# Kernel optimization log

Measured on AMD Instinct MI355X. Metric: run time of the kernel, lower is better.

The kernel has to match this reference:

```python
import jax, jax.numpy as jnp
import numpy as np
import math

B, C, N, T = 16, 32, 500, 10
NH, DK = 8, 8
D = NH * DK  # 64
TT = 6       # tem_size after conv_temp1 (10->6)
EPS = 1e-5


def setup_inputs() -> dict:
    key = jax.random.key(0)
    ks = jax.random.split(key, 32)
    s = 0.05
    rn = lambda k, shp: jax.random.normal(k, shp, dtype=jnp.float32) * s
    return {
        "x": jax.random.normal(ks[0], (B, C, N, T), dtype=jnp.float32),
        "A": jax.random.uniform(ks[1], (N, N), dtype=jnp.float32) / N,
        "conv1_W": rn(ks[2], (32, 32)), "conv1_b": jnp.zeros((32,), jnp.float32),
        "te1_W": rn(ks[3], (64, 32)), "te1_b": jnp.zeros((64,), jnp.float32),
        "convq_W": rn(ks[4], (64, 64, 1, 3)), "convq_b": jnp.zeros((64,), jnp.float32),
        "convk_W": rn(ks[5], (64, 64, 1, 3)), "convk_b": jnp.zeros((64,), jnp.float32),
        "linv_W": rn(ks[6], (64, 64)), "linv_b": jnp.zeros((64,), jnp.float32),
        "lino_W": rn(ks[7], (64, 64)), "lino_b": jnp.zeros((64,), jnp.float32),
        "te2_W": rn(ks[8], (32, 64)), "te2_b": jnp.zeros((32,), jnp.float32),
        "mlp_W": rn(ks[9], (64, 160)), "mlp_b": jnp.zeros((64,), jnp.float32),
        "ct1_W": rn(ks[10], (6, 10)), "ct1_b": jnp.zeros((6,), jnp.float32),
        "tat_c1_W": rn(ks[11], (32,)), "tat_c2_W": rn(ks[12], (500,)),
        "tat_w": rn(ks[13], (500, 32)), "tat_b": jnp.zeros((6, 6), jnp.float32),
        "tat_v": rn(ks[14], (6, 6)),
        "bn1_g": jnp.ones((6,), jnp.float32), "bn1_b": jnp.zeros((6,), jnp.float32),
        "bn2_g": jnp.ones((32,), jnp.float32), "bn2_b": jnp.zeros((32,), jnp.float32),
    }


def _forward(x, A, conv1_W, conv1_b, te1_W, te1_b, convq_W, convq_b, convk_W, convk_b,
             linv_W, linv_b, lino_W, lino_b, te2_W, te2_b, mlp_W, mlp_b, ct1_W, ct1_b,
             tat_c1_W, tat_c2_W, tat_w, tat_b, tat_v, bn1_g, bn1_b, bn2_g, bn2_b):
    b, c, n, t = x.shape
    c1x1 = lambda z, W, bb: jnp.einsum('bchw,oc->bohw', z, W) + bb[None, :, None, None]
    residual = c1x1(x, conv1_W, conv1_b)                      # (B,32,N,T)
    h = c1x1(x, te1_W, te1_b)                                 # (B,64,N,T)
    # --- temporal-context multi-head self-attention (att bias is 0 in source due to bug) ---
    dn = ('NCHW', 'OIHW', 'NCHW')
    q = jax.lax.conv_general_dilated(h, convq_W, (1, 1), ((0, 0), (1, 1)), dimension_numbers=dn) + convq_b[None, :, None, None]
    k = jax.lax.conv_general_dilated(h, convk_W, (1, 1), ((0, 0), (1, 1)), dimension_numbers=dn) + convk_b[None, :, None, None]
    sh = lambda z: z.reshape(b, NH, DK, n, t).transpose(0, 3, 1, 4, 2)  # (B,N,h,T,dk)
    q, k = sh(q), sh(k)
    hp = h.transpose(0, 2, 3, 1)                              # (B,N,T,64)
    v = (hp @ linv_W.T + linv_b).reshape(b, n, t, NH, DK).transpose(0, 1, 3, 2, 4)
    p = jax.nn.softmax(jnp.einsum('bnhtd,bnhsd->bnhts', q, k) / math.sqrt(DK), axis=-1)
    o = jnp.einsum('bnhts,bnhsd->bnhtd', p, v).transpose(0, 1, 3, 2, 4).reshape(b, n, t, D)
    h = (o @ lino_W.T + lino_b).transpose(0, 3, 1, 2)         # (B,64,N,T)
    h = c1x1(h, te2_W, te2_b)                                 # (B,32,N,T)
    # --- multi_gcn_d: static adjacency diffusion + per-timestep attention adjacency ---
    co = h.shape[1]
    xt = h.transpose(0, 3, 2, 1)                              # (B,T,N,C)
    att = jax.nn.softmax(jnp.einsum('btnc,btmc->btnm', xt, xt) / math.sqrt(co), axis=-1)
    outs = [h]
    z = jnp.einsum('btvc,wv->btwc', xt, A); outs.append(z.transpose(0, 3, 2, 1))
    z = jnp.einsum('btvc,wv->btwc', z, A);  outs.append(z.transpose(0, 3, 2, 1))
    z = jnp.einsum('btvc,btwv->btwc', xt, att); outs.append(z.transpose(0, 3, 2, 1))
    z = jnp.einsum('btvc,btwv->btwc', z, att);  outs.append(z.transpose(0, 3, 2, 1))
    hc = c1x1(jnp.concatenate(outs, axis=1), mlp_W, mlp_b)    # (B,64,N,T)
    g = jnp.tanh(hc[:, :co]) * jax.nn.sigmoid(hc[:, co:])     # (B,32,N,10)
    # --- conv_temp1: 1x1 conv over the time axis, 10 -> 6 ---
    g = jnp.einsum('bcnt,st->bcns', g, ct1_W) + ct1_b[None, None, None, :]  # (B,32,N,6)
    # --- TATT_1 temporal attention coefficients ---
    f1 = jnp.einsum('bcnt,c->btn', g, tat_c1_W)               # (B,6,N)
    f2 = jnp.einsum('bcnt,n->bct', g, tat_c2_W)               # (B,32,6)
    logits = jax.nn.sigmoid(jnp.einsum('btn,nc,bcs->bts', f1, tat_w, f2) + tat_b)
    logits = jnp.einsum('pt,bts->bps', tat_v, logits)         # (B,6,6)
    lp = logits.transpose(0, 2, 1)
    mu = lp.mean((0, 2), keepdims=True); var = lp.var((0, 2), keepdims=True)
    lp = (lp - mu) / jnp.sqrt(var + EPS) * bn1_g[None, :, None] + bn1_b[None, :, None]
    coefs = jax.nn.softmax(lp.transpose(0, 2, 1), axis=-1)    # (B,6,6)
    Tc = coefs.transpose(0, 2, 1)
    xo = jnp.einsum('bcnl,blq->bcnq', g, Tc)                  # (B,32,N,6)
    xo = jnp.where(xo > 0, xo, 0.01 * xo) + residual[..., -xo.shape[-1]:]
    mu = xo.mean((0, 2, 3), keepdims=True); var = xo.var((0, 2, 3), keepdims=True)
    return (xo - mu) / jnp.sqrt(var + EPS) * bn2_g[None, :, None, None] + bn2_b[None, :, None, None]


def reference(x, A, conv1_W, conv1_b, te1_W, te1_b, convq_W, convq_b, convk_W, convk_b,
              linv_W, linv_b, lino_W, lino_b, te2_W, te2_b, mlp_W, mlp_b, ct1_W, ct1_b,
              tat_c1_W, tat_c2_W, tat_w, tat_b, tat_v, bn1_g, bn1_b, bn2_g, bn2_b):
    return _forward(x, A, conv1_W, conv1_b, te1_W, te1_b, convq_W, convq_b, convk_W, convk_b,
                    linv_W, linv_b, lino_W, lino_b, te2_W, te2_b, mlp_W, mlp_b, ct1_W, ct1_b,
                    tat_c1_W, tat_c2_W, tat_w, tat_b, tat_v, bn1_g, bn1_b, bn2_g, bn2_b)
```

## Files before the change

### kernel.cpp

```cpp
#include <hip/hip_runtime.h>

typedef unsigned short u16;
typedef unsigned int u32;

__device__ __forceinline__ float b2f(u16 v) { return __uint_as_float((u32)v << 16); }
__device__ __forceinline__ float lopart(u32 u) { return __uint_as_float(u << 16); }
__device__ __forceinline__ float hipart(u32 u) { return __uint_as_float(u & 0xffff0000u); }
__device__ __forceinline__ u16 f2b(float f) {
  u32 u = __float_as_uint(f);
  u32 r = u + 0x7fffu + ((u >> 16) & 1u);
  return (u16)(r >> 16);
}
__device__ __forceinline__ u32 pk2(float a, float b) {
  return (u32)f2b(a) | ((u32)f2b(b) << 16);
}
__device__ __forceinline__ u32 cvtpk(float lo, float hi) {
  u32 r;
  asm("v_cvt_pk_bf16_f32 %0, %1, %2" : "=v"(r) : "v"(lo), "v"(hi));
  return r;
}
__device__ __forceinline__ float rd(const void* p, int i, bool BF) {
  return BF ? b2f(((const u16*)p)[i]) : ((const float*)p)[i];
}

struct Ptrs { const void* p[29]; };

typedef __attribute__((ext_vector_type(8))) short short8;
typedef __attribute__((ext_vector_type(4))) float floatx4;

__global__ __launch_bounds__(256) void k_prep(Ptrs ps, float* __restrict__ Wf,
                                              u16* __restrict__ Abf, float* __restrict__ WT,
                                              u16* __restrict__ WBu, float* __restrict__ stats) {
  bool BF = ((*(const u32*)ps.p[25]) & 0xffffu) != 0;
  int blk = blockIdx.x, tid = threadIdx.x;
  if (blk < 256) {
    int j = blk * 256 + tid;
    if (j >= 65322) return;
    const int SZ[27] = {1024,32,2048,64,12288,64,12288,64,4096,64,4096,64,2048,32,
                        10240,64,60,6,32,500,16000,36,36,6,6,32,32};
    int t = 0, off = 0;
#pragma unroll
    for (int k = 0; k < 27; ++k) {
      if (t == k && j >= off + SZ[k]) { off += SZ[k]; t = k + 1; }
    }
    Wf[j] = rd(ps.p[2 + t], j - off, BF);
  } else if (blk < 1280) {
    int i = (blk - 256) * 256 + tid;
    int r = i >> 9, v = i & 511;
    bool in = (r < 500) && (v < 500);
    u16 o = 0;
    if (in) o = BF ? ((const u16*)ps.p[1])[r * 500 + v] : f2b(((const float*)ps.p[1])[r * 500 + v]);
    Abf[i] = o;
  } else if (blk < 1366) {
    int i = (blk - 1280) * 256 + tid;
    const void* p2  = ps.p[2];
    const void* p4  = ps.p[4];
    const void* p5  = ps.p[5];
    const void* p6  = ps.p[6];
    const void* p7  = ps.p[7];
    const void* p8  = ps.p[8];
    const void* p9  = ps.p[9];
    const void* p10 = ps.p[10];
    const void* p11 = ps.p[11];
    const void* p12 = ps.p[12];
    const void* p13 = ps.p[13];
    const void* p14 = ps.p[14];
    const void* p15 = ps.p[15];
    const void* p16 = ps.p[16];
    if (i < 1024) {
      WT[i] = rd(p2, (i & 31) * 32 + (i >> 5), BF);
    } else if (i < 7168) {
      int j2 = i - 1024;
      int o = j2 & 63, ct = j2 >> 6;
      int c = ct / 3, tap = ct - c * 3;
      float sq = 0.f, sk = 0.f;
      for (int i2 = 0; i2 < 64; ++i2) {
        float te = rd(p4, i2 * 32 + c, BF);
        sq += rd(p6, o * 192 + i2 * 3 + tap, BF) * te;
        sk += rd(p8, o * 192 + i2 * 3 + tap, BF) * te;
      }
      ((u32*)WT)[i] = pk2(sq, sk);
    } else if (i < 7552) {
      int j2 = i - 7168;
      int f = j2 >> 6, o = j2 & 63;
      const void* pw = (f & 1) ? p8 : p6;
      float S0 = 0.f, S1 = 0.f, S2 = 0.f;
      for (int i2 = 0; i2 < 64; ++i2) {
        float tb = rd(p5, i2, BF);
        S0 += rd(pw, o * 192 + i2 * 3 + 0, BF) * tb;
        S1 += rd(pw, o * 192 + i2 * 3 + 1, BF) * tb;
        S2 += rd(pw, o * 192 + i2 * 3 + 2, BF) * tb;
      }
      float r;
      if (f == 0)      r = rd(p7, o, BF) + S0 + S1 + S2;
      else if (f == 1) r = rd(p9, o, BF) + S0 + S1 + S2;
      else if (f < 4)  r = S0;
      else             r = S2;
      WT[i] = r;
    } else if (i < 9600) {
      int j2 = i - 7552;
      int c = j2 >> 6, o = j2 & 63;
      float s = 0.f;
      for (int i2 = 0; i2 < 64; ++i2)
        s += rd(p10, o * 64 + i2, BF) * rd(p4, i2 * 32 + c, BF);
      WT[i] = s;
    } else if (i < 9664) {
      int o = i - 9600;
      float s = rd(p11, o, BF);
      for (int i2 = 0; i2 < 64; ++i2)
        s += rd(p10, o * 64 + i2, BF) * rd(p5, i2, BF);
      WT[i] = s;
    } else if (i < 11712) {
      int j2 = i - 9664;
      int jj = j2 >> 5, c = j2 & 31;
      float s = 0.f;
      for (int o2 = 0; o2 < 64; ++o2)
        s += rd(p14, c * 64 + o2, BF) * rd(p12, o2 * 64 + jj, BF);
      WT[i] = s;
    } else if (i < 11744) {
      int c = i - 11712;
      float s = rd(p15, c, BF);
      for (int o2 = 0; o2 < 64; ++o2)
        s += rd(p14, c * 64 + o2, BF) * rd(p13, o2, BF);
      WT[i] = s;
    } else if (i < 21984) {
      int j2 = i - 11744;
      int j = j2 & 7, lanev = (j2 >> 3) & 63, ct = (j2 >> 9) & 3, kt = j2 >> 11;
      int qv = lanev >> 4, lnv = lanev & 15;
      int o = ct * 16 + lnv, k = kt * 32 + qv * 8 + j;
      WBu[j2] = f2b(rd(p16, o * 160 + k, BF));
    }
  } else {
    if (tid < 64) stats[tid] = 0.f;
  }
}

__global__ __launch_bounds__(256, 4) void k_a2m(const u16* __restrict__ Abf,
                                                u16* __restrict__ A2bf) {
  __shared__ u32 blsT[8192];
  int tid = threadIdx.x;
  int c0 = blockIdx.x * 32;
  for (int i = tid; i < 8192; i += 256) {
    int c = i & 31, h = i >> 5;
    int r0 = 2 * h;
    u32 lo = Abf[r0 * 512 + c0 + c];
    u32 hi = Abf[(r0 + 1) * 512 + c0 + c];
    blsT[c * 256 + (((h & 0xFC) ^ ((c & 15) << 2)) | (h & 3))] = lo | (hi << 16);
  }
  __syncthreads();
  int lane = tid & 63, wave = tid >> 6;
  int q = lane >> 4, ln = lane & 15;
  int rbase = blockIdx.y * 64 + wave * 16;
  const u32* Au = (const u32*)Abf;
  int arow = (rbase + ln) * 256;
  union F8 { u32 u[4]; short8 s; };
  floatx4 acc[2] = {{0.f,0.f,0.f,0.f},{0.f,0.f,0.f,0.f}};
  for (int c2 = 0; c2 < 16; ++c2) {
    int hb = c2 * 16 + q * 4;
    F8 af;
#pragma unroll
    for (int i2 = 0; i2 < 4; ++i2) af.u[i2] = Au[arow + hb + i2];
#pragma unroll
    for (int t2 = 0; t2 < 2; ++t2) {
      int c = t2 * 16 + ln;
      int baseT = c * 256 + (hb ^ ((c & 15) << 2));
      F8 bf;
#pragma unroll
      for (int i2 = 0; i2 < 4; ++i2) bf.u[i2] = blsT[baseT + i2];
      acc[t2] = __builtin_amdgcn_mfma_f32_16x16x32_bf16(af.s, bf.s, acc[t2], 0, 0, 0);
    }
  }
#pragma unroll
  for (int t2 = 0; t2 < 2; ++t2) {
#pragma unroll
    for (int i2 = 0; i2 < 4; ++i2) {
      int r = rbase + q * 4 + i2;
      A2bf[r * 512 + c0 + t2 * 16 + ln] = f2b(acc[t2][i2]);
    }
  }
}

__global__ __launch_bounds__(256, 7) void k_front3(
    const void* __restrict__ xraw, const void* __restrict__ g1, const float* __restrict__ WT,
    const float* __restrict__ c1B,
    float* __restrict__ h3x, float* __restrict__ res6)
{
  __shared__ __align__(16) float arena[4][1440];
  int tid = threadIdx.x;
  int wave = tid >> 6, lane = tid & 63;
  float* Aw = arena[wave];
  int pair = blockIdx.x * 4 + wave;
  int b = pair / 500, n = pair - b * 500;

  const float* c1T  = WT;
  const u32*   qkF  = (const u32*)(WT + 1024);
  const float* bCq  = WT + 7168;
  const float* bCk  = WT + 7232;
  const float* bE0q = WT + 7296;
  const float* bE0k = WT + 7360;
  const float* bE2q = WT + 7424;
  const float* bE2k = WT + 7488;
  const float* vT   = WT + 7552;
  const float* bvp  = WT + 9600;
  const float* otT  = WT + 9664;
  const float* botp = WT + 11712;

  {
    bool BF = ((*(const u32*)g1) & 0xffffu) != 0;
    int c0 = lane >> 1, hf = (lane & 1) * 5;
    int base = ((b * 32 + c0) * 500 + n) * 10 + hf;
    float* dst = Aw + c0 * 12 + hf;
    if (BF) {
      const u16* xp = (const u16*)xraw + base;
#pragma unroll
      for (int k2 = 0; k2 < 5; ++k2) dst[k2] = b2f(xp[k2]);
    } else {
      const float* xp = (const float*)xraw + base;
#pragma unroll
      for (int k2 = 0; k2 < 5; ++k2) dst[k2] = xp[k2];
    }
  }
  __builtin_amdgcn_wave_barrier();

  int cl = lane & 31, th = lane >> 5;

  {
    float r0 = c1B[cl], r1 = r0, r2 = r0;
#pragma unroll 4
    for (int i = 0; i < 32; ++i) {
      float w = c1T[i * 32 + cl];
      const float* xr = Aw + i * 12 + 4 + th * 3;
      r0 += w * xr[0]; r1 += w * xr[1]; r2 += w * xr[2];
    }
    float* rp = res6 + ((b * 32 + cl) * 500 + n) * 6 + th * 3;
    rp[0] = r0; rp[1] = r1; rp[2] = r2;
  }

  float qr[10], kr[10], vr[10];
  {
    float cq = bCq[lane], ck = bCk[lane], bv = bvp[lane];
#pragma unroll
    for (int t = 0; t < 10; ++t) { qr[t] = cq; kr[t] = ck; vr[t] = bv; }
    qr[0] -= bE0q[lane]; kr[0] -= bE0k[lane];
    qr[9] -= bE2q[lane]; kr[9] -= bE2k[lane];
    const u32* qp0 = qkF + lane;
    const float* vp0 = vT + lane;
#pragma unroll 2
    for (int c = 0; c < 32; ++c) {
      const float* xr = Aw + c * 12;
      float4 ha = *(const float4*)xr;
      float4 hb = *(const float4*)(xr + 4);
      float2 hc = *(const float2*)(xr + 8);
      u32 u0 = qp0[c * 192];
      u32 u1 = qp0[c * 192 + 64];
      u32 u2 = qp0[c * 192 + 128];
      float wv = vp0[c * 64];
      float q0 = lopart(u0), q1 = lopart(u1), q2 = lopart(u2);
      float k0 = hipart(u0), k1 = hipart(u1), k2v = hipart(u2);
      float hh[10] = {ha.x, ha.y, ha.z, ha.w, hb.x, hb.y, hb.z, hb.w, hc.x, hc.y};
#pragma unroll
      for (int t = 0; t < 10; ++t) { float c_ = hh[t]; qr[t] += q1 * c_; kr[t] += k1 * c_; vr[t] += wv * c_; }
#pragma unroll
      for (int t = 1; t < 10; ++t) { float c_ = hh[t - 1]; qr[t] += q0 * c_; kr[t] += k0 * c_; }
#pragma unroll
      for (int t = 0; t < 9; ++t) { float c_ = hh[t + 1]; qr[t] += q2 * c_; kr[t] += k2v * c_; }
    }
  }
  __builtin_amdgcn_wave_barrier();
  {
    u32* qu = (u32*)Aw + lane * 5;
    u32* ku = (u32*)Aw + 320 + lane * 5;
#pragma unroll
    for (int m = 0; m < 5; ++m) {
      qu[m] = cvtpk(qr[2 * m], qr[2 * m + 1]);
      ku[m] = cvtpk(kr[2 * m], kr[2 * m + 1]);
    }
  }
  __builtin_amdgcn_wave_barrier();

  {
    const u32* qb = (const u32*)Aw;
    const u32* kb = (const u32*)Aw + 320;
#pragma unroll
    for (int pass = 0; pass < 2; ++pass) {
      int row = pass * 64 + lane;
      if (row < 80) {
        int h8 = (row / 10) * 8, r = row - (row / 10) * 10;
        int rm = r >> 1, rs = r & 1;
        float sv[10];
#pragma unroll
        for (int s = 0; s < 10; ++s) sv[s] = 0.f;
#pragma unroll 2
        for (int d = 0; d < 8; ++d) {
          int jj = h8 + d;
          u32 qu = qb[jj * 5 + rm];
          float qv = rs ? hipart(qu) : lopart(qu);
          const u32* kp2 = kb + jj * 5;
          u32 ka0 = kp2[0], ka1 = kp2[1], ka2 = kp2[2], ka3 = kp2[3], ka4 = kp2[4];
          sv[0] += qv * lopart(ka0); sv[1] += qv * hipart(ka0);
          sv[2] += qv * lopart(ka1); sv[3] += qv * hipart(ka1);
          sv[4] += qv * lopart(ka2); sv[5] += qv * hipart(ka2);
          sv[6] += qv * lopart(ka3); sv[7] += qv * hipart(ka3);
          sv[8] += qv * lopart(ka4); sv[9] += qv * hipart(ka4);
        }
        const float sc_ = 0.35355339059327373f;
        float mx = sv[0];
#pragma unroll
        for (int s = 1; s < 10; ++s) mx = fmaxf(mx, sv[s]);
        float tot = 0.f, ev[10];
#pragma unroll
        for (int s = 0; s < 10; ++s) { ev[s] = expf((sv[s] - mx) * sc_); tot += ev[s]; }
        float inv = 1.f / tot;
        float* pp = Aw + 640 + row * 10;
#pragma unroll
        for (int s = 0; s < 10; ++s) pp[s] = ev[s] * inv;
      }
    }
  }
  __builtin_amdgcn_wave_barrier();

  {
    const float* pb = Aw + 640 + (lane >> 3) * 100;
    float orr[10];
#pragma unroll
    for (int t = 0; t < 10; ++t) {
      const float* pr = pb + t * 10;
      float a = 0.f;
#pragma unroll
      for (int s = 0; s < 10; ++s) a += pr[s] * vr[s];
      orr[t] = a;
    }
    float* op = Aw + lane * 12;
    *(float4*)op       = make_float4(orr[0], orr[1], orr[2], orr[3]);
    *(float4*)(op + 4) = make_float4(orr[4], orr[5], orr[6], orr[7]);
    *(float2*)(op + 8) = make_float2(orr[8], orr[9]);
  }
  __builtin_amdgcn_wave_barrier();

  {
    float bt2 = botp[cl];
    float a5[5];
#pragma unroll
    for (int k2 = 0; k2 < 5; ++k2) a5[k2] = bt2;
    const float* tp0 = otT + cl;
    const float* base = Aw + th * 5;
#pragma unroll 2
    for (int j = 0; j < 64; ++j) {
      float w = tp0[j * 32];
      const float* lp = base + j * 12;
#pragma unroll
      for (int k2 = 0; k2 < 5; ++k2) a5[k2] += w * lp[k2];
    }
    int t0 = th * 5;
#pragma unroll
    for (int k2 = 0; k2 < 5; ++k2)
      h3x[((b * 10 + t0 + k2) * 500 + n) * 32 + cl] = a5[k2];
  }
}

__global__ __launch_bounds__(256, 4) void k_z12m(const float* __restrict__ h3x,
    const u16* __restrict__ Abf, const u16* __restrict__ A2bf,
    float* __restrict__ z1x, float* __restrict__ z2x) {
  __shared__ u32 xlsT[8192];
  int tid = threadIdx.x, bt = blockIdx.x;
  const float* src = h3x + bt * 16000;
  for (int i = tid; i < 8192; i += 256) {
    int n = i & 31, h = i >> 5;
    int r0 = 2 * h;
    float v0 = (r0 < 500) ? src[r0 * 32 + n] : 0.f;
    float v1 = (r0 + 1 < 500) ? src[(r0 + 1) * 32 + n] : 0.f;
    xlsT[n * 256 + (((h & 0xFC) ^ ((n & 15) << 2)) | (h & 3))] = cvtpk(v0, v1);
  }
  __syncthreads();
  int lane = tid & 63, wave = tid >> 6;
  int q = lane >> 4, ln = lane & 15;
  int rbase = blockIdx.y * 64 + wave * 16;
  const u32* Au = (const u32*)Abf;
  const u32* A2u = (const u32*)A2bf;
  int arow = (rbase + ln) * 256;
  union F8 { u32 u[4]; short8 s; };
  floatx4 acc1[2] = {{0.f,0.f,0.f,0.f},{0.f,0.f,0.f,0.f}};
  floatx4 acc2[2] = {{0.f,0.f,0.f,0.f},{0.f,0.f,0.f,0.f}};
  for (int c2 = 0; c2 < 16; ++c2) {
    int hb = c2 * 16 + q * 4;
    F8 a1f, a2f;
#pragma unroll
    for (int i2 = 0; i2 < 4; ++i2) {
      a1f.u[i2] = Au[arow + hb + i2];
      a2f.u[i2] = A2u[arow + hb + i2];
    }
#pragma unroll
    for (int t2 = 0; t2 < 2; ++t2) {
      int n = t2 * 16 + ln;
      int baseT = n * 256 + (hb ^ ((n & 15) << 2));
      F8 bf;
#pragma unroll
      for (int i2 = 0; i2 < 4; ++i2) bf.u[i2] = xlsT[baseT + i2];
      acc1[t2] = __builtin_amdgcn_mfma_f32_16x16x32_bf16(a1f.s, bf.s, acc1[t2], 0, 0, 0);
      acc2[t2] = __builtin_amdgcn_mfma_f32_16x16x32_bf16(a2f.s, bf.s, acc2[t2], 0, 0, 0);
    }
  }
  int outb = bt * 16000;
#pragma unroll
  for (int t2 = 0; t2 < 2; ++t2) {
#pragma unroll
    for (int i2 = 0; i2 < 4; ++i2) {
      int r = rbase + q * 4 + i2;
      if (r < 500) {
        z1x[outb + r * 32 + t2 * 16 + ln] = acc1[t2][i2];
        z2x[outb + r * 32 + t2 * 16 + ln] = acc2[t2][i2];
      }
    }
  }
}

__global__ __launch_bounds__(256, 3) void k_attn2(const float* __restrict__ keys,
                                                  const float* __restrict__ vals,
                                                  float* __restrict__ outp) {
  __shared__ u32 xls[10240];
  __shared__ u32 aux[1280];
  int tid = threadIdx.x, bt = blockIdx.x;
  const float* kb = keys + bt * 16000;
  const float* vb = vals + bt * 16000;
  for (int i = tid; i < 8192; i += 256) {
    int r = i >> 4, cu = i & 15;
    float2 g = make_float2(0.f, 0.f);
    if (r < 500) g = *(const float2*)(kb + r * 32 + cu * 2);
    xls[r * 20 + cu] = cvtpk(g.x, g.y);
  }
  u32 vreg[32];
#pragma unroll
  for (int j = 0; j < 32; ++j) {
    int i = tid + j * 256;
    int n = i & 31, h = i >> 5;
    int r0 = 2 * h;
    float v0 = (r0 < 500) ? vb[r0 * 32 + n] : 0.f;
    float v1 = (r0 + 1 < 500) ? vb[(r0 + 1) * 32 + n] : 0.f;
    vreg[j] = cvtpk(v0, v1);
  }
  __syncthreads();
  int lane = tid & 63, wave = tid >> 6;
  int q = lane >> 4, ln = lane & 15;
  int wrow = wave >> 1, ch = wave & 1;
  int rbase = blockIdx.y * 32 + wrow * 16;
  float* smx = (float*)aux;
  float* sms = smx + 64;
  u32* myp = aux + 128 + wave * 272;
  float* zex = (float*)aux;
  union F8 { u32 u[4]; short8 s; };
  F8 af;
  {
    int r = rbase + ln;
    int wbase = r * 20 + q * 4;
#pragma unroll
    for (int i2 = 0; i2 < 4; ++i2)
      af.u[i2] = xls[wbase + i2];
  }
  floatx4 acc[16];
#pragma unroll
  for (int ctl = 0; ctl < 16; ++ctl) {
    int r2 = (ch * 16 + ctl) * 16 + ln;
    int wb2 = r2 * 20 + q * 4;
    F8 bf;
#pragma unroll
    for (int i2 = 0; i2 < 4; ++i2)
      bf.u[i2] = xls[wb2 + i2];
    acc[ctl] = __builtin_amdgcn_mfma_f32_16x16x32_bf16(af.s, bf.s,
              (floatx4){0.f, 0.f, 0.f, 0.f}, 0, 0, 0);
  }
  if (ch == 1 && ln >= 4) {
#pragma unroll
    for (int i2 = 0; i2 < 4; ++i2) acc[15][i2] = -1e30f;
  }
  const float sc = 0.17677669529663687f;
  float m[4];
#pragma unroll
  for (int i2 = 0; i2 < 4; ++i2) {
    float mm = -1e30f;
#pragma unroll
    for (int ctl = 0; ctl < 16; ++ctl) mm = fmaxf(mm, acc[ctl][i2]);
#pragma unroll
    for (int d = 1; d < 16; d <<= 1) mm = fmaxf(mm, __shfl_xor(mm, d));
    m[i2] = mm;
  }
  if (ln == 0) {
#pragma unroll
    for (int i2 = 0; i2 < 4; ++i2) smx[wave * 16 + q * 4 + i2] = m[i2];
  }
  __syncthreads();
  float sp[4];
#pragma unroll
  for (int i2 = 0; i2 < 4; ++i2) {
    float mm = fmaxf(m[i2], smx[(wave ^ 1) * 16 + q * 4 + i2]);
    float s = 0.f;
#pragma unroll
    for (int ctl = 0; ctl < 16; ++ctl) {
      float e = __expf((acc[ctl][i2] - mm) * sc);
      acc[ctl][i2] = e; s += e;
    }
#pragma unroll
    for (int d = 1; d < 16; d <<= 1) s += __shfl_xor(s, d);
    sp[i2] = s;
  }
  if (ln == 0) {
#pragma unroll
    for (int i2 = 0; i2 < 4; ++i2) sms[wave * 16 + q * 4 + i2] = sp[i2];
  }
#pragma unroll
  for (int j = 0; j < 32; ++j) {
    int i = tid + j * 256;
    int n = i & 31, h = i >> 5;
    xls[n * 256 + (((h & 0xFC) ^ ((n & 15) << 2)) | (h & 3))] = vreg[j];
  }
  __syncthreads();
  float inv[4];
#pragma unroll
  for (int i2 = 0; i2 < 4; ++i2)
    inv[i2] = 1.f / (sp[i2] + sms[(wave ^ 1) * 16 + q * 4 + i2]);
  floatx4 zacc[2] = {{0.f,0.f,0.f,0.f},{0.f,0.f,0.f,0.f}};
  u16* pw = (u16*)myp;
  for (int c2l = 0; c2l < 8; ++c2l) {
#pragma unroll
    for (int t2 = 0; t2 < 2; ++t2) {
      int ctl = c2l * 2 + t2;
#pragma unroll
      for (int i2 = 0; i2 < 4; ++i2)
        pw[(q * 4 + i2) * 34 + t2 * 16 + ln] = f2b(acc[ctl][i2]);
    }
    __builtin_amdgcn_wave_barrier();
    F8 pa;
#pragma unroll
    for (int i2 = 0; i2 < 4; ++i2) pa.u[i2] = myp[ln * 17 + q * 4 + i2];
    int hb = (ch * 8 + c2l) * 16 + q * 4;
#pragma unroll
    for (int t2 = 0; t2 < 2; ++t2) {
      int n = t2 * 16 + ln;
      int baseT = n * 256 + (hb ^ ((n & 15) << 2));
      F8 bf;
#pragma unroll
      for (int i2 = 0; i2 < 4; ++i2) bf.u[i2] = xls[baseT + i2];
      zacc[t2] = __builtin_amdgcn_mfma_f32_16x16x32_bf16(pa.s, bf.s, zacc[t2], 0, 0, 0);
    }
    __builtin_amdgcn_wave_barrier();
  }
  __syncthreads();
  if (ch) {
#pragma unroll
    for (int t2 = 0; t2 < 2; ++t2)
#pragma unroll
      for (int i2 = 0; i2 < 4; ++i2)
        zex[wrow * 544 + (q * 4 + i2) * 34 + t2 * 16 + ln] = zacc[t2][i2];
  }
  __syncthreads();
  if (!ch) {
    int outb = bt * 16000;
#pragma unroll
    for (int t2 = 0; t2 < 2; ++t2) {
#pragma unroll
      for (int i2 = 0; i2 < 4; ++i2) {
        int r = rbase + q * 4 + i2;
        if (r < 500) {
          float vsum = zacc[t2][i2] + zex[wrow * 544 + (q * 4 + i2) * 34 + t2 * 16 + ln];
          outp[outb + r * 32 + t2 * 16 + ln] = vsum * inv[i2];
        }
      }
    }
  }
}

__global__ __launch_bounds__(256, 2) void k_gate(
    const float* __restrict__ h3x, const float* __restrict__ z1x, const float* __restrict__ z2x,
    const float* __restrict__ z3x, const float* __restrict__ z4x,
    const u32* __restrict__ WBq, const float* __restrict__ mlpB,
    const float* __restrict__ ct1W, const float* __restrict__ ct1B,
    float* __restrict__ g2w)
{
  __shared__ u32 wlds[5120];
  int tid = threadIdx.x;
  for (int i = tid; i < 5120; i += 256) wlds[i] = WBq[i];
  __syncthreads();
  int lane = tid & 63, wave = tid >> 6;
  int q = lane >> 4, ln = lane & 15;
  int b = blockIdx.y;
  int n0 = blockIdx.x * 32 + wave * 8;
  int nA = n0 + (ln & 7);
  int tAb = ln >> 3;
  int nD = n0 + (q & 1) * 4;
  int tDb = q >> 1;
  float g2a[4][2][6];
#pragma unroll
  for (int i = 0; i < 4; ++i)
#pragma unroll
    for (int ch = 0; ch < 2; ++ch)
#pragma unroll
      for (int s = 0; s < 6; ++s) g2a[i][ch][s] = 0.f;
  float bias[4];
#pragma unroll
  for (int ct = 0; ct < 4; ++ct) bias[ct] = mlpB[ct * 16 + ln];
  union F8 { u32 u[4]; short8 s; };
  for (int tile = 0; tile < 5; ++tile) {
    int tA = tile * 2 + tAb;
    int offA = (((b * 10 + tA) * 500) + nA) * 32 + q * 8;
    floatx4 acc[4];
#pragma unroll
    for (int ct = 0; ct < 4; ++ct) acc[ct] = (floatx4){bias[ct], bias[ct], bias[ct], bias[ct]};
#pragma unroll
    for (int kt = 0; kt < 5; ++kt) {
      const float* sp = kt == 0 ? h3x : kt == 1 ? z1x : kt == 2 ? z2x : kt == 3 ? z3x : z4x;
      float4 a0 = *(const float4*)(sp + offA);
      float4 a1 = *(const float4*)(sp + offA + 4);
      F8 af;
      af.u[0] = cvtpk(a0.x, a0.y);
      af.u[1] = cvtpk(a0.z, a0.w);
      af.u[2] = cvtpk(a1.x, a1.y);
      af.u[3] = cvtpk(a1.z, a1.w);
#pragma unroll
      for (int ct = 0; ct < 4; ++ct) {
        F8 bfr;
        const u32* wp = wlds + (((kt * 4 + ct) << 6) + lane) * 4;
#pragma unroll
        for (int i2 = 0; i2 < 4; ++i2) bfr.u[i2] = wp[i2];
        acc[ct] = __builtin_amdgcn_mfma_f32_16x16x32_bf16(af.s, bfr.s, acc[ct], 0, 0, 0);
      }
    }
    int tD = tile * 2 + tDb;
    float c6[6];
#pragma unroll
    for (int s = 0; s < 6; ++s) c6[s] = ct1W[s * 10 + tD];
#pragma unroll
    for (int i = 0; i < 4; ++i) {
      float e0 = __expf(2.f * acc[0][i]);
      float g0 = ((e0 - 1.f) / (e0 + 1.f)) * (1.f / (1.f + __expf(-acc[2][i])));
      float e1 = __expf(2.f * acc[1][i]);
      float g1 = ((e1 - 1.f) / (e1 + 1.f)) * (1.f / (1.f + __expf(-acc[3][i])));
#pragma unroll
      for (int s = 0; s < 6; ++s) {
        g2a[i][0][s] += g0 * c6[s];
        g2a[i][1][s] += g1 * c6[s];
      }
    }
  }
#pragma unroll
  for (int i = 0; i < 4; ++i)
#pragma unroll
    for (int ch = 0; ch < 2; ++ch)
#pragma unroll
      for (int s = 0; s < 6; ++s)
        g2a[i][ch][s] += __shfl_xor(g2a[i][ch][s], 32);
  if (q < 2) {
#pragma unroll
    for (int i = 0; i < 4; ++i) {
      int n = nD + i;
      if (n < 500) {
#pragma unroll
        for (int ch = 0; ch < 2; ++ch) {
          int c = ln + ch * 16;
          float* gp = g2w + ((b * 32 + c) * 500 + n) * 6;
#pragma unroll
          for (int s = 0; s < 6; ++s) gp[s] = g2a[i][ch][s] + ct1B[s];
        }
      }
    }
  }
}

__global__ __launch_bounds__(256) void k_f12(const float* __restrict__ g2w,
                                             const float* __restrict__ tc1W,
                                             const float* __restrict__ c2W,
                                             float* __restrict__ f1w, float* __restrict__ f2w) {
  int blk = blockIdx.x, tid = threadIdx.x;
  if (blk < 188) {
    int i = blk * 256 + tid;
    if (i >= 48000) return;
    int b = i / 3000, rem = i - b * 3000, s = rem / 500, n = rem - s * 500;
    float a = 0.f;
    for (int c = 0; c < 32; ++c) a += g2w[((b * 32 + c) * 500 + n) * 6 + s] * tc1W[c];
    f1w[(b * 6 + s) * 500 + n] = a;
  } else {
    int pb = (blk - 188) * 4 + (tid >> 6);
    int b = pb >> 5, c = pb & 31, lane = tid & 63;
    float acc[6];
#pragma unroll
    for (int t = 0; t < 6; ++t) acc[t] = 0.f;
    for (int n = lane; n < 500; n += 64) {
      float w = c2W[n];
      const float* gp = g2w + ((b * 32 + c) * 500 + n) * 6;
#pragma unroll
      for (int t = 0; t < 6; ++t) acc[t] += w * gp[t];
    }
#pragma unroll
    for (int t = 0; t < 6; ++t)
      for (int off = 32; off; off >>= 1) acc[t] += __shfl_xor(acc[t], off);
    if (lane == 0) {
#pragma unroll
      for (int t = 0; t < 6; ++t) f2w[(b * 32 + c) * 6 + t] = acc[t];
    }
  }
}

__global__ __launch_bounds__(256) void k_tatt(
    const float* __restrict__ f1w, const float* __restrict__ tatw,
    const float* __restrict__ f2w, const float* __restrict__ tatb, const float* __restrict__ tatv,
    float* __restrict__ lg2w)
{
  __shared__ float mid[192];
  __shared__ float lgt[36];
  int b = blockIdx.x, tid = threadIdx.x;
  if (tid < 192) {
    int t = tid >> 5, c = tid & 31;
    float a = 0.f;
    const float* f1p = f1w + (b * 6 + t) * 500;
    for (int n = 0; n < 500; ++n) a += f1p[n] * tatw[n * 32 + c];
    mid[t * 32 + c] = a;
  }
  __syncthreads();
  if (tid < 36) {
    int t = tid / 6, s = tid - t * 6;
    float a = tatb[t * 6 + s];
    for (int c = 0; c < 32; ++c) a += mid[t * 32 + c] * f2w[(b * 32 + c) * 6 + s];
    lgt[t * 6 + s] = 1.f / (1.f + expf(-a));
  }
  __syncthreads();
  if (tid < 36) {
    int p = tid / 6, s = tid - p * 6;
    float a = 0.f;
#pragma unroll
    for (int t2 = 0; t2 < 6; ++t2) a += tatv[p * 6 + t2] * lgt[t2 * 6 + s];
    lg2w[(b * 6 + p) * 6 + s] = a;
  }
}

__global__ __launch_bounds__(128) void k_coefs(const float* __restrict__ lg2w,
    const float* __restrict__ bn1g, const float* __restrict__ bn1b, float* __restrict__ tcw) {
  __shared__ float mu[6], iv[6], gg[6], bb[6];
  int tid = threadIdx.x;
  if (tid < 6) {
    float s = 0.f, sq = 0.f;
    for (int b = 0; b < 16; ++b)
      for (int q = 0; q < 6; ++q) {
        float v = lg2w[(b * 6 + q) * 6 + tid];
        s += v; sq += v * v;
      }
    float m = s / 96.f;
    mu[tid] = m;
    iv[tid] = rsqrtf(sq / 96.f - m * m + 1e-5f);
    gg[tid] = bn1g[tid]; bb[tid] = bn1b[tid];
  }
  __syncthreads();
  for (int idx = tid; idx < 96; idx += 128) {
    int b = idx / 6, q = idx - b * 6;
    float v[6], mx = -1e30f;
#pragma unroll
    for (int l = 0; l < 6; ++l) {
      v[l] = (lg2w[(b * 6 + q) * 6 + l] - mu[l]) * iv[l] * gg[l] + bb[l];
      mx = fmaxf(mx, v[l]);
    }
    float tot = 0.f;
#pragma unroll
    for (int l = 0; l < 6; ++l) { v[l] = expf(v[l] - mx); tot += v[l]; }
    float inv = 1.f / tot;
#pragma unroll
    for (int l = 0; l < 6; ++l) tcw[(b * 6 + l) * 6 + q] = v[l] * inv;
  }
}

__global__ __launch_bounds__(256) void k_xo(const float* __restrict__ g2w,
    const float* __restrict__ res6, const float* __restrict__ tcw,
    float* __restrict__ xow, float* __restrict__ stats) {
  __shared__ float Tcl[36];
  __shared__ float redS[32][8], redQ[32][8];
  int b = blockIdx.x, chunk = blockIdx.y, tid = threadIdx.x;
  if (tid < 36) Tcl[tid] = tcw[b * 36 + tid];
  __syncthreads();
  int c = tid & 31, sub = tid >> 5;
  int n0 = chunk * 50;
  float s = 0.f, sq = 0.f;
  for (int idx = sub; idx < 300; idx += 8) {
    int nl = idx / 6, q = idx - nl * 6;
    int n = n0 + nl;
    int base = ((b * 32 + c) * 500 + n) * 6;
    const float* gp = g2w + base;
    float xv = 0.f;
#pragma unroll
    for (int l = 0; l < 6; ++l) xv += gp[l] * Tcl[l * 6 + q];
    xv = xv > 0.f ? xv : 0.01f * xv;
    xv += res6[base + q];
    xow[base + q] = xv;
    s += xv; sq += xv * xv;
  }
  redS[c][sub] = s; redQ[c][sub] = sq;
  __syncthreads();
  if (sub == 0) {
    float ts = 0.f, tq = 0.f;
#pragma unroll
    for (int k = 0; k < 8; ++k) { ts += redS[c][k]; tq += redQ[c][k]; }
    atomicAdd(&stats[c], ts);
    atomicAdd(&stats[32 + c], tq);
  }
}

__global__ __launch_bounds__(256) void k_out(const float* __restrict__ xow,
    const float* __restrict__ stats, const float* __restrict__ g2c, const float* __restrict__ b2c,
    float* __restrict__ out) {
  int base = (blockIdx.x * 256 + threadIdx.x) * 4;
#pragma unroll
  for (int k = 0; k < 4; ++k) {
    int i = base + k;
    int c = (i / 3000) & 31;
    float m = stats[c] * (1.f / 48000.f);
    float var = stats[32 + c] * (1.f / 48000.f) - m * m;
    out[i] = (xow[i] - m) * rsqrtf(var + 1e-5f) * g2c[c] + b2c[c];
  }
}

extern "C" void kernel_launch(void* const* d_in, const int* in_sizes, int n_in,
                              void* d_out, int out_size, void* d_ws, size_t ws_size,
                              hipStream_t stream)
{
  (void)in_sizes; (void)out_size;

  float* ws = (float*)d_ws;
  float* Af   = ws;
  float* Wf   = Af + 250000;
  float* A2   = Wf + 65536;
  float* h3x  = A2 + 250000;
  float* z1x  = h3x + 2560000;
  float* z2x  = z1x + 2560000;
  float* z3x  = z2x + 2560000;
  float* z4x  = z3x + 2560000;
  float* res6 = z4x + 2560000;
  float* g2w  = res6 + 1536000;
  float* f1w  = g2w + 1536000;
  float* f2w  = f1w + 48000;
  float* lg2w = f2w + 3072;
  float* tcw  = lg2w + 576;
  float* stats= tcw + 576;
  float* xow  = z1x;
  u16*   Abf  = (u16*)g2w;
  u16*   A2bf = (u16*)(g2w + 131072);
  float* WTp  = g2w + 262144;
  u16*   WBu  = (u16*)f1w;
  if (ws_size < (size_t)16489952 * sizeof(float)) return;

  const float* c1B  = Wf + 1024;
  const float* mlpB = Wf + 48512;
  const float* ct1W = Wf + 48576;
  const float* ct1B = Wf + 48636;
  const float* tc1W = Wf + 48642;
  const float* tc2W = Wf + 48674;
  const float* tatw = Wf + 49174;
  const float* tatb = Wf + 65174;
  const float* tatv = Wf + 65210;
  const float* bn1g = Wf + 65246;
  const float* bn1b = Wf + 65252;
  const float* bn2g = Wf + 65258;
  const float* bn2b = Wf + 65290;

  Ptrs ps;
  for (int i = 0; i < 29; ++i) ps.p[i] = (i < n_in) ? d_in[i] : d_in[0];

  k_prep <<<dim3(1367),    256, 0, stream>>>(ps, Wf, Abf, WTp, WBu, stats);
  k_a2m  <<<dim3(16, 8),   256, 0, stream>>>(Abf, A2bf);
  k_front3<<<dim3(2000),   256, 0, stream>>>(ps.p[0], ps.p[25], WTp, c1B, h3x, res6);
  k_z12m <<<dim3(160, 8),  256, 0, stream>>>(h3x, Abf, A2bf, z1x, z2x);
  k_attn2<<<dim3(160, 16), 256, 0, stream>>>(h3x, h3x, z3x);
  k_attn2<<<dim3(160, 16), 256, 0, stream>>>(h3x, z3x, z4x);
  k_gate <<<dim3(16, 16),  256, 0, stream>>>(h3x, z1x, z2x, z3x, z4x,
                                             (const u32*)WBu, mlpB, ct1W, ct1B, g2w);
  k_f12  <<<dim3(316),     256, 0, stream>>>(g2w, tc1W, tc2W, f1w, f2w);
  k_tatt <<<dim3(16),      256, 0, stream>>>(f1w, tatw, f2w, tatb, tatv, lg2w);
  k_coefs<<<dim3(1),       128, 0, stream>>>(lg2w, bn1g, bn1b, tcw);
  k_xo   <<<dim3(16, 10),  256, 0, stream>>>(g2w, res6, tcw, xow, stats);
  k_out  <<<dim3(1500),    256, 0, stream>>>(xow, stats, bn2g, bn2b, (float*)d_out);
}
```

Before: 410.5 us.

## Reuse staged keys/values across eight query chunks per attention block

The attention kernel now loads keys and values into LDS once per block, stored as separate buffers, and then loops over eight 32-row query chunks. Previously every 32-row query tile reloaded and converted all 500 keys and values. The grid shrinks from 16 to 2 blocks in y, which cuts redundant global loads and bf16 conversions. In exchange LDS use grows, occupancy drops to 2 blocks per CU, and only 320 blocks are launched, so there is less parallelism and latency hiding.

```diff
diff --git a/kernel.cpp b/kernel.cpp
--- a/kernel.cpp
+++ b/kernel.cpp
@@ -414,154 +414,146 @@
   }
 }
 
-__global__ __launch_bounds__(256, 3) void k_attn2(const float* __restrict__ keys,
+__global__ __launch_bounds__(256, 2) void k_attn2(const float* __restrict__ keys,
                                                   const float* __restrict__ vals,
                                                   float* __restrict__ outp) {
-  __shared__ u32 xls[10240];
-  __shared__ u32 aux[1280];
-  int tid = threadIdx.x, bt = blockIdx.x;
+  __shared__ u32 kls[10240];
+  __shared__ u32 vls[8192];
+  __shared__ u32 aux[1216];
+  int tid = threadIdx.x, bt = blockIdx.x, yh = blockIdx.y;
   const float* kb = keys + bt * 16000;
   const float* vb = vals + bt * 16000;
   for (int i = tid; i < 8192; i += 256) {
     int r = i >> 4, cu = i & 15;
     float2 g = make_float2(0.f, 0.f);
     if (r < 500) g = *(const float2*)(kb + r * 32 + cu * 2);
-    xls[r * 20 + cu] = cvtpk(g.x, g.y);
-  }
-  u32 vreg[32];
-#pragma unroll
-  for (int j = 0; j < 32; ++j) {
-    int i = tid + j * 256;
+    kls[r * 20 + cu] = cvtpk(g.x, g.y);
     int n = i & 31, h = i >> 5;
     int r0 = 2 * h;
     float v0 = (r0 < 500) ? vb[r0 * 32 + n] : 0.f;
     float v1 = (r0 + 1 < 500) ? vb[(r0 + 1) * 32 + n] : 0.f;
-    vreg[j] = cvtpk(v0, v1);
+    vls[n * 256 + (((h & 0xFC) ^ ((n & 15) << 2)) | (h & 3))] = cvtpk(v0, v1);
   }
   __syncthreads();
   int lane = tid & 63, wave = tid >> 6;
   int q = lane >> 4, ln = lane & 15;
   int wrow = wave >> 1, ch = wave & 1;
-  int rbase = blockIdx.y * 32 + wrow * 16;
-  float* smx = (float*)aux;
-  float* sms = smx + 64;
-  u32* myp = aux + 128 + wave * 272;
+  float* smx = (float*)(aux + 1088);
+  float* sms = (float*)(aux + 1152);
+  u32* myp = aux + wave * 272;
   float* zex = (float*)aux;
+  u16* pw = (u16*)myp;
   union F8 { u32 u[4]; short8 s; };
-  F8 af;
-  {
-    int r = rbase + ln;
-    int wbase = r * 20 + q * 4;
+  const float sc = 0.17677669529663687f;
+  int outb = bt * 16000;
+  for (int chunk = 0; chunk < 8; ++chunk) {
+    int rbase = yh * 256 + chunk * 32 + wrow * 16;
+    F8 af;
+    {
+      int r = rbase + ln;
+      int wbase = r * 20 + q * 4;
+#pragma unroll
+      for (int i2 = 0; i2 < 4; ++i2)
+        af.u[i2] = kls[wbase + i2];
+    }
+    floatx4 acc[16];
+#pragma unroll
+    for (int ctl = 0; ctl < 16; ++ctl) {
+      int r2 = (ch * 16 + ctl) * 16 + ln;
+      int wb2 = r2 * 20 + q * 4;
+      F8 bf;
+#pragma unroll
+      for (int i2 = 0; i2 < 4; ++i2)
+        bf.u[i2] = kls[wb2 + i2];
+      acc[ctl] = __builtin_amdgcn_mfma_f32_16x16x32_bf16(af.s, bf.s,
+                (floatx4){0.f, 0.f, 0.f, 0.f}, 0, 0, 0);
+    }
+    if (ch == 1 && ln >= 4) {
+#pragma unroll
+      for (int i2 = 0; i2 < 4; ++i2) acc[15][i2] = -1e30f;
+    }
+    float m[4];
+#pragma unroll
+    for (int i2 = 0; i2 < 4; ++i2) {
+      float mm = -1e30f;
+#pragma unroll
+      for (int ctl = 0; ctl < 16; ++ctl) mm = fmaxf(mm, acc[ctl][i2]);
+#pragma unroll
+      for (int d = 1; d < 16; d <<= 1) mm = fmaxf(mm, __shfl_xor(mm, d));
+      m[i2] = mm;
+    }
+    if (ln == 0) {
+#pragma unroll
+      for (int i2 = 0; i2 < 4; ++i2) smx[wave * 16 + q * 4 + i2] = m[i2];
+    }
+    __syncthreads();
+    float sp[4];
+#pragma unroll
+    for (int i2 = 0; i2 < 4; ++i2) {
+      float mm = fmaxf(m[i2], smx[(wave ^ 1) * 16 + q * 4 + i2]);
+      float s = 0.f;
+#pragma unroll
+      for (int ctl = 0; ctl < 16; ++ctl) {
+        float e = __expf((acc[ctl][i2] - mm) * sc);
+        acc[ctl][i2] = e; s += e;
+      }
+#pragma unroll
+      for (int d = 1; d < 16; d <<= 1) s += __shfl_xor(s, d);
+      sp[i2] = s;
+    }
+    if (ln == 0) {
+#pragma unroll
+      for (int i2 = 0; i2 < 4; ++i2) sms[wave * 16 + q * 4 + i2] = sp[i2];
+    }
+    __syncthreads();
+    float inv[4];
 #pragma unroll
     for (int i2 = 0; i2 < 4; ++i2)
-      af.u[i2] = xls[wbase + i2];
-  }
-  floatx4 acc[16];
-#pragma unroll
-  for (int ctl = 0; ctl < 16; ++ctl) {
-    int r2 = (ch * 16 + ctl) * 16 + ln;
-    int wb2 = r2 * 20 + q * 4;
-    F8 bf;
-#pragma unroll
-    for (int i2 = 0; i2 < 4; ++i2)
-      bf.u[i2] = xls[wb2 + i2];
-    acc[ctl] = __builtin_amdgcn_mfma_f32_16x16x32_bf16(af.s, bf.s,
-              (floatx4){0.f, 0.f, 0.f, 0.f}, 0, 0, 0);
-  }
-  if (ch == 1 && ln >= 4) {
-#pragma unroll
-    for (int i2 = 0; i2 < 4; ++i2) acc[15][i2] = -1e30f;
-  }
-  const float sc = 0.17677669529663687f;
-  float m[4];
-#pragma unroll
-  for (int i2 = 0; i2 < 4; ++i2) {
-    float mm = -1e30f;
-#pragma unroll
-    for (int ctl = 0; ctl < 16; ++ctl) mm = fmaxf(mm, acc[ctl][i2]);
-#pragma unroll
-    for (int d = 1; d < 16; d <<= 1) mm = fmaxf(mm, __shfl_xor(mm, d));
-    m[i2] = mm;
-  }
-  if (ln == 0) {
-#pragma unroll
-    for (int i2 = 0; i2 < 4; ++i2) smx[wave * 16 + q * 4 + i2] = m[i2];
-  }
-  __syncthreads();
-  float sp[4];
-#pragma unroll
-  for (int i2 = 0; i2 < 4; ++i2) {
-    float mm = fmaxf(m[i2], smx[(wave ^ 1) * 16 + q * 4 + i2]);
-    float s = 0.f;
-#pragma unroll
-    for (int ctl = 0; ctl < 16; ++ctl) {
-      float e = __expf((acc[ctl][i2] - mm) * sc);
-      acc[ctl][i2] = e; s += e;
-    }
-#pragma unroll
-    for (int d = 1; d < 16; d <<= 1) s += __shfl_xor(s, d);
-    sp[i2] = s;
-  }
-  if (ln == 0) {
-#pragma unroll
-    for (int i2 = 0; i2 < 4; ++i2) sms[wave * 16 + q * 4 + i2] = sp[i2];
-  }
-#pragma unroll
-  for (int j = 0; j < 32; ++j) {
-    int i = tid + j * 256;
-    int n = i & 31, h = i >> 5;
-    xls[n * 256 + (((h & 0xFC) ^ ((n & 15) << 2)) | (h & 3))] = vreg[j];
-  }
-  __syncthreads();
-  float inv[4];
-#pragma unroll
-  for (int i2 = 0; i2 < 4; ++i2)
-    inv[i2] = 1.f / (sp[i2] + sms[(wave ^ 1) * 16 + q * 4 + i2]);
-  floatx4 zacc[2] = {{0.f,0.f,0.f,0.f},{0.f,0.f,0.f,0.f}};
-  u16* pw = (u16*)myp;
-  for (int c2l = 0; c2l < 8; ++c2l) {
-#pragma unroll
-    for (int t2 = 0; t2 < 2; ++t2) {
-      int ctl = c2l * 2 + t2;
-#pragma unroll
-      for (int i2 = 0; i2 < 4; ++i2)
-        pw[(q * 4 + i2) * 34 + t2 * 16 + ln] = f2b(acc[ctl][i2]);
-    }
-    __builtin_amdgcn_wave_barrier();
-    F8 pa;
-#pragma unroll
-    for (int i2 = 0; i2 < 4; ++i2) pa.u[i2] = myp[ln * 17 + q * 4 + i2];
-    int hb = (ch * 8 + c2l) * 16 + q * 4;
-#pragma unroll
-    for (int t2 = 0; t2 < 2; ++t2) {
-      int n = t2 * 16 + ln;
-      int baseT = n * 256 + (hb ^ ((n & 15) << 2));
-      F8 bf;
-#pragma unroll
-      for (int i2 = 0; i2 < 4; ++i2) bf.u[i2] = xls[baseT + i2];
-      zacc[t2] = __builtin_amdgcn_mfma_f32_16x16x32_bf16(pa.s, bf.s, zacc[t2], 0, 0, 0);
-    }
-    __builtin_amdgcn_wave_barrier();
-  }
-  __syncthreads();
-  if (ch) {
-#pragma unroll
-    for (int t2 = 0; t2 < 2; ++t2)
-#pragma unroll
-      for (int i2 = 0; i2 < 4; ++i2)
-        zex[wrow * 544 + (q * 4 + i2) * 34 + t2 * 16 + ln] = zacc[t2][i2];
-  }
-  __syncthreads();
-  if (!ch) {
-    int outb = bt * 16000;
-#pragma unroll
-    for (int t2 = 0; t2 < 2; ++t2) {
-#pragma unroll
-      for (int i2 = 0; i2 < 4; ++i2) {
-        int r = rbase + q * 4 + i2;
-        if (r < 500) {
-          float vsum = zacc[t2][i2] + zex[wrow * 544 + (q * 4 + i2) * 34 + t2 * 16 + ln];
-          outp[outb + r * 32 + t2 * 16 + ln] = vsum * inv[i2];
+      inv[i2] = 1.f / (sp[i2] + sms[(wave ^ 1) * 16 + q * 4 + i2]);
+    floatx4 zacc[2] = {{0.f,0.f,0.f,0.f},{0.f,0.f,0.f,0.f}};
+    for (int c2l = 0; c2l < 8; ++c2l) {
+#pragma unroll
+      for (int t2 = 0; t2 < 2; ++t2) {
+        int ctl = c2l * 2 + t2;
+#pragma unroll
+        for (int i2 = 0; i2 < 4; ++i2)
+          pw[(q * 4 + i2) * 34 + t2 * 16 + ln] = f2b(acc[ctl][i2]);
+      }
+      __builtin_amdgcn_wave_barrier();
+      F8 pa;
+#pragma unroll
+      for (int i2 = 0; i2 < 4; ++i2) pa.u[i2] = myp[ln * 17 + q * 4 + i2];
+      int hb = (ch * 8 + c2l) * 16 + q * 4;
+#pragma unroll
+      for (int t2 = 0; t2 < 2; ++t2) {
+        int n = t2 * 16 + ln;
+        int baseT = n * 256 + (hb ^ ((n & 15) << 2));
+        F8 bf;
+#pragma unroll
+        for (int i2 = 0; i2 < 4; ++i2) bf.u[i2] = vls[baseT + i2];
+        zacc[t2] = __builtin_amdgcn_mfma_f32_16x16x32_bf16(pa.s, bf.s, zacc[t2], 0, 0, 0);
+      }
+      __builtin_amdgcn_wave_barrier();
+    }
+    __syncthreads();
+    if (ch) {
+#pragma unroll
+      for (int t2 = 0; t2 < 2; ++t2)
+#pragma unroll
+        for (int i2 = 0; i2 < 4; ++i2)
+          zex[wrow * 544 + (q * 4 + i2) * 34 + t2 * 16 + ln] = zacc[t2][i2];
+    }
+    __syncthreads();
+    if (!ch) {
+#pragma unroll
+      for (int t2 = 0; t2 < 2; ++t2) {
+#pragma unroll
+        for (int i2 = 0; i2 < 4; ++i2) {
+          int r = rbase + q * 4 + i2;
+          if (r < 500) {
+            float vsum = zacc[t2][i2] + zex[wrow * 544 + (q * 4 + i2) * 34 + t2 * 16 + ln];
+            outp[outb + r * 32 + t2 * 16 + ln] = vsum * inv[i2];
+          }
         }
       }
     }
@@ -863,8 +855,8 @@
   k_a2m  <<<dim3(16, 8),   256, 0, stream>>>(Abf, A2bf);
   k_front3<<<dim3(2000),   256, 0, stream>>>(ps.p[0], ps.p[25], WTp, c1B, h3x, res6);
   k_z12m <<<dim3(160, 8),  256, 0, stream>>>(h3x, Abf, A2bf, z1x, z2x);
-  k_attn2<<<dim3(160, 16), 256, 0, stream>>>(h3x, h3x, z3x);
-  k_attn2<<<dim3(160, 16), 256, 0, stream>>>(h3x, z3x, z4x);
+  k_attn2<<<dim3(160, 2),  256, 0, stream>>>(h3x, h3x, z3x);
+  k_attn2<<<dim3(160, 2),  256, 0, stream>>>(h3x, z3x, z4x);
   k_gate <<<dim3(16, 16),  256, 0, stream>>>(h3x, z1x, z2x, z3x, z4x,
                                              (const u32*)WBu, mlpB, ct1W, ct1B, g2w);
   k_f12  <<<dim3(316),     256, 0, stream>>>(g2w, tc1W, tc2W, f1w, f2w);
```

Result: no change. 406.8 us (-0.9%).
